# Performance work log

Measured on AMD Instinct MI355X. Metric: run time of the kernel, lower is better.

The kernel has to match this reference:

```python
import jax, jax.numpy as jnp
import numpy as np

B, C, R = 8, 256, 14
H_HEADS = 4
KD = 16            # key_dim
D_V = 64           # attn_ratio * key_dim
KS = 5             # dw conv kernel
N = R * R * R      # tokens


def _bias_idx():
    # replicate original offset logic: only first two coords (|dx|,|dy|) used
    pts = np.array(np.meshgrid(np.arange(R), np.arange(R), np.arange(R), indexing='ij'))
    pts = pts.reshape(3, -1).T  # (N, 3) in itertools.product order
    dx = np.abs(pts[:, 0:1] - pts[None, :, 0])  # (N, N)
    dy = np.abs(pts[:, 1:2] - pts[None, :, 1])
    return (dx * R + dy).astype(np.int32)  # (N, N), values in [0, R*R)


def setup_inputs() -> dict:
    key = jax.random.key(0)
    ks = jax.random.split(key, 12)
    cph = C // H_HEADS
    qkv_out = 2 * KD + D_V
    inp = {
        'x': jax.random.normal(ks[0], (B, C, R, R, R), jnp.float32),
        'Wqkv': jax.random.normal(ks[1], (H_HEADS, qkv_out, cph), jnp.float32) * 0.05,
        'qkv_scale': 1.0 + 0.05 * jax.random.normal(ks[2], (H_HEADS, qkv_out), jnp.float32),
        'qkv_bias': 0.05 * jax.random.normal(ks[3], (H_HEADS, qkv_out), jnp.float32),
        'Wdw': jax.random.normal(ks[4], (H_HEADS, KD, 1, KS, KS, KS), jnp.float32) * 0.05,
        'dw_scale': 1.0 + 0.05 * jax.random.normal(ks[5], (H_HEADS, KD), jnp.float32),
        'dw_bias': 0.05 * jax.random.normal(ks[6], (H_HEADS, KD), jnp.float32),
        'Wproj': jax.random.normal(ks[7], (C, D_V * H_HEADS), jnp.float32) * 0.02,
        'proj_scale': 1.0 + 0.05 * jax.random.normal(ks[8], (C,), jnp.float32),
        'proj_bias': 0.05 * jax.random.normal(ks[9], (C,), jnp.float32),
        'attention_biases': 0.02 * jax.random.normal(ks[10], (H_HEADS, R * R), jnp.float32),
        'bias_idx': jnp.asarray(_bias_idx()),
    }
    return inp


def reference(x, Wqkv, qkv_scale, qkv_bias, Wdw, dw_scale, dw_bias,
              Wproj, proj_scale, proj_bias, attention_biases, bias_idx):
    scale = KD ** (-0.5)
    ab = attention_biases[:, bias_idx]  # (h, N, N) relative-position bias gather
    feats_in = jnp.split(x, H_HEADS, axis=1)  # h x (B, C/h, R, R, R)
    dn = ('NCDHW', 'OIDHW', 'NCDHW')
    feats_out = []
    feat = feats_in[0]
    for i in range(H_HEADS):
        if i > 0:
            feat = feat + feats_in[i]
        # 1x1x1 conv QKV + fused BN (inference-style scale/shift)
        y = jnp.einsum('oc,bcxyz->boxyz', Wqkv[i], feat)
        y = y * qkv_scale[i][:, None, None, None] + qkv_bias[i][:, None, None, None]
        q = y[:, :KD]
        k = y[:, KD:2 * KD]
        v = y[:, 2 * KD:]
        # depthwise conv on q + fused BN
        q = jax.lax.conv_general_dilated(q, Wdw[i], (1, 1, 1), 'SAME',
                                         feature_group_count=KD, dimension_numbers=dn)
        q = q * dw_scale[i][:, None, None, None] + dw_bias[i][:, None, None, None]
        qf = q.reshape(B, KD, N)
        kf = k.reshape(B, KD, N)
        vf = v.reshape(B, D_V, N)
        attn = jnp.einsum('bcn,bcm->bnm', qf, kf) * scale + ab[i]  # (B, N, N)
        attn = jax.nn.softmax(attn, axis=-1)
        feat = jnp.einsum('bcm,bnm->bcn', vf, attn).reshape(B, D_V, R, R, R)
        feats_out.append(feat)
    h = jax.nn.relu(jnp.concatenate(feats_out, axis=1))  # (B, d*h, R, R, R)
    out = jnp.einsum('oc,bcxyz->boxyz', Wproj, h)
    out = out * proj_scale[:, None, None, None] + proj_bias[:, None, None, None]
    return out
```

## Files before the change

### kernel.cpp

```cpp
#include <hip/hip_runtime.h>

#define B_    8
#define C_    256
#define R_    14
#define R2    196
#define N3    2744
#define NP    2752
#define NH    4
#define KD    16
#define DV    64
#define QKVO  96
#define MT    64
#define NTILE 43
#define SPLIT 4
#define TPC   11

#define SC2   0.36067376f
#define LOG2E 1.44269504f

typedef __attribute__((ext_vector_type(8))) short short8v;
typedef __attribute__((ext_vector_type(4))) short short4v;
typedef __attribute__((ext_vector_type(4))) float float4v;

__device__ __forceinline__ int iabs(int v){ return v < 0 ? -v : v; }

__device__ __forceinline__ short f2bf(float f){
    union { float f; unsigned int u; } c; c.f = f;
    return (short)((c.u + 0x7FFFu + ((c.u >> 16) & 1u)) >> 16);
}
__device__ __forceinline__ float bf2f(short s){
    union { unsigned int u; float f; } c; c.u = ((unsigned int)(unsigned short)s) << 16;
    return c.f;
}

__global__ __launch_bounds__(256)
void wprep_kernel(const float* __restrict__ Wp, short* __restrict__ whi,
                  short* __restrict__ wlo, const float* __restrict__ Wqkv,
                  const float* __restrict__ qsc, short* __restrict__ wqhi,
                  short* __restrict__ wqlo)
{
    int i = blockIdx.x * 256 + threadIdx.x;
    {
        float w = Wp[i];
        short hi = f2bf(w);
        short lo = f2bf(w - bf2f(hi));
        whi[i] = hi; wlo[i] = lo;
    }
    if (i < NH * QKVO * 64) {
        int o_all = i >> 6;
        float w = Wqkv[i] * qsc[o_all];
        short hi = f2bf(w);
        short lo = f2bf(w - bf2f(hi));
        wqhi[i] = hi; wqlo[i] = lo;
    }
}

__global__ __launch_bounds__(256, 2)
void qkv_mfma(const float* __restrict__ x, float* __restrict__ h,
              const float* __restrict__ pacc, const float* __restrict__ pl,
              const short* __restrict__ wqhi, const short* __restrict__ wqlo,
              const float* __restrict__ qbi,
              float* __restrict__ q0, short* __restrict__ kbf, short* __restrict__ vbf,
              int head)
{
    __shared__ short fhi[64][72];
    __shared__ short flo[64][72];
    __shared__ float bsh[96];
    __shared__ float linv_s[64];

    const int b = blockIdx.y;
    const int n0 = blockIdx.x * 64;
    const int t = threadIdx.x;
    const int w = t >> 6, l = t & 63, g = l >> 4, ln = l & 15;

    if (t < 96) bsh[t] = qbi[head * QKVO + t];

    if (head > 0) {
        if (t < 64) {
            int n = n0 + t;
            float lt = pl[(size_t)(b * SPLIT + 0) * NP + n]
                     + pl[(size_t)(b * SPLIT + 1) * NP + n]
                     + pl[(size_t)(b * SPLIT + 2) * NP + n]
                     + pl[(size_t)(b * SPLIT + 3) * NP + n];
            linv_s[t] = 1.f / lt;
        }
        __syncthreads();
    }

    {
        const int sc_ = t & 63;
        const int sng = (t >> 6) * 16;
        const int nb = n0 + sng;
        const float* xs = x + ((size_t)b * C_ + head * DV + sc_) * N3 + nb;
        float fv[16];
        const bool fullblk = (nb + 15 < N3);
        if (fullblk) {
#pragma unroll
            for (int e4 = 0; e4 < 4; e4++) {
                float4 xv = ((const float4*)xs)[e4];
                fv[4*e4+0] = xv.x; fv[4*e4+1] = xv.y; fv[4*e4+2] = xv.z; fv[4*e4+3] = xv.w;
            }
        } else {
#pragma unroll
            for (int e = 0; e < 16; e++) fv[e] = (nb + e < N3) ? xs[e] : 0.f;
        }
        if (head > 0) {
            const float* pb = pacc + (size_t)b * SPLIT * DV * NP + (size_t)sc_ * NP + nb;
            float* hw = h + ((size_t)b * C_ + (head - 1) * DV + sc_) * N3 + nb;
            const size_t zs = (size_t)DV * NP;
            if (fullblk) {
#pragma unroll
                for (int e4 = 0; e4 < 4; e4++) {
                    float4 a0 = ((const float4*)(pb         ))[e4];
                    float4 a1 = ((const float4*)(pb +     zs))[e4];
                    float4 a2 = ((const float4*)(pb + 2 * zs))[e4];
                    float4 a3 = ((const float4*)(pb + 3 * zs))[e4];
                    float hc[4];
                    hc[0] = (a0.x + a1.x + a2.x + a3.x) * linv_s[sng + 4*e4 + 0];
                    hc[1] = (a0.y + a1.y + a2.y + a3.y) * linv_s[sng + 4*e4 + 1];
                    hc[2] = (a0.z + a1.z + a2.z + a3.z) * linv_s[sng + 4*e4 + 2];
                    hc[3] = (a0.w + a1.w + a2.w + a3.w) * linv_s[sng + 4*e4 + 3];
                    *(float4*)&hw[4*e4] = make_float4(hc[0], hc[1], hc[2], hc[3]);
                    fv[4*e4+0] += hc[0]; fv[4*e4+1] += hc[1];
                    fv[4*e4+2] += hc[2]; fv[4*e4+3] += hc[3];
                }
            } else {
#pragma unroll
                for (int e = 0; e < 16; e++) {
                    if (nb + e < N3) {
                        float a = pb[e] + pb[e + zs] + pb[e + 2*zs] + pb[e + 3*zs];
                        float hc = a * linv_s[sng + e];
                        hw[e] = hc;
                        fv[e] += hc;
                    }
                }
            }
        }
#pragma unroll
        for (int e = 0; e < 16; e++) {
            short hi = f2bf(fv[e]);
            short lo = f2bf(fv[e] - bf2f(hi));
            fhi[sng + e][sc_] = hi;
            flo[sng + e][sc_] = lo;
        }
    }
    __syncthreads();

    float4v acc[6];
#pragma unroll
    for (int os = 0; os < 6; os++) acc[os] = (float4v){0.f, 0.f, 0.f, 0.f};

    const short* wqh = wqhi + head * QKVO * 64;
    const short* wql = wqlo + head * QKVO * 64;
#pragma unroll
    for (int ck = 0; ck < 2; ck++) {
        short8v bh = *(const short8v*)&fhi[w * 16 + ln][ck * 32 + g * 8];
        short8v bl = *(const short8v*)&flo[w * 16 + ln][ck * 32 + g * 8];
#pragma unroll
        for (int os = 0; os < 6; os++) {
            size_t off = (size_t)(os * 16 + ln) * 64 + ck * 32 + g * 8;
            short8v wh = *(const short8v*)(wqh + off);
            short8v wl = *(const short8v*)(wql + off);
            acc[os] = __builtin_amdgcn_mfma_f32_16x16x32_bf16(wh, bh, acc[os], 0, 0, 0);
            acc[os] = __builtin_amdgcn_mfma_f32_16x16x32_bf16(wh, bl, acc[os], 0, 0, 0);
            acc[os] = __builtin_amdgcn_mfma_f32_16x16x32_bf16(wl, bh, acc[os], 0, 0, 0);
        }
    }

    const int n_ = n0 + w * 16 + ln;
    const bool ok = n_ < N3;
    float* qo = q0 + (size_t)b * KD * NP;
    short* ko = kbf + (size_t)b * NP * 16 + (size_t)n_ * 16;
    short* vo = vbf + (size_t)b * DV * NP;
#pragma unroll
    for (int os = 0; os < 6; os++) {
#pragma unroll
        for (int r = 0; r < 4; r++) {
            int o = os * 16 + g * 4 + r;
            float y = ok ? acc[os][r] + bsh[o] : 0.f;
            if (o < KD)            qo[(size_t)o * NP + n_] = y;
            else if (o < 2 * KD)   ko[o - KD] = f2bf(y);
            else                   vo[(size_t)(o - 2 * KD) * NP + n_] = f2bf(y);
        }
    }
}

__global__ __launch_bounds__(256)
void dwconv_kernel(float* __restrict__ q0, const float* __restrict__ Wdw,
                   const float* __restrict__ dsc, const float* __restrict__ dbi,
                   int head)
{
    __shared__ float pv[18 * 18 * 18];
    int b = blockIdx.y, c = blockIdx.x;
    int t = threadIdx.x;
    float* qc = q0 + ((size_t)b * KD + c) * NP;

    for (int i = t; i < 5832; i += 256) pv[i] = 0.f;
    __syncthreads();
    for (int i = t; i < N3; i += 256) {
        int xx = i / R2; int rem = i - xx * R2; int yy = rem / R_; int zz = rem - yy * R_;
        pv[(xx + 2) * 324 + (yy + 2) * 18 + (zz + 2)] = qc[i];
    }
    __syncthreads();

    const float* w = Wdw + (head * KD + c) * 125;
    float scl = dsc[head * KD + c], bia = dbi[head * KD + c];

    if (t < R2) {
        int x = t / R_, y = t - (t / R_) * R_;
        float acc[14];
#pragma unroll
        for (int z = 0; z < 14; z++) acc[z] = 0.f;
#pragma unroll
        for (int a = 0; a < 5; a++) {
#pragma unroll
            for (int bb = 0; bb < 5; bb++) {
                const float* base = &pv[(x + a) * 324 + (y + bb) * 18];
                float col[18];
#pragma unroll
                for (int j = 0; j < 18; j++) col[j] = base[j];
#pragma unroll
                for (int cc = 0; cc < 5; cc++) {
                    float wv = w[a * 25 + bb * 5 + cc];
#pragma unroll
                    for (int z = 0; z < 14; z++) acc[z] += wv * col[z + cc];
                }
            }
        }
        float* qo = qc + x * R2 + y * R_;
#pragma unroll
        for (int z = 0; z < 14; z++) qo[z] = acc[z] * scl + bia;
    }
}

__global__ __launch_bounds__(256, 6)
void attn_partial(const float* __restrict__ q0, const short* __restrict__ kbf,
                  const short* __restrict__ vbf, float* __restrict__ pacc,
                  float* __restrict__ pl, const float* __restrict__ abias, int head)
{
    __shared__ short ktT[64][40];
    __shared__ short vtT[64][72];
    __shared__ short plds[4][16][72];
    __shared__ int   mja[64];
    __shared__ float patch[6][8];

    const int b = blockIdx.y, z = blockIdx.z;
    const int qbase = blockIdx.x * 64;
    const int t = threadIdx.x;
    const int w = t >> 6;
    const int l = t & 63;
    const int g = l >> 4;
    const int ln = l & 15;

    const float* abh = abias + head * R2;
    const float* qq  = q0  + (size_t)b * KD * NP;
    const short* kbs = kbf + (size_t)b * NP * 16;
    const short* vbs = vbf + (size_t)b * DV * NP;

    {
        int mm = t & 63, dg = t >> 6;
        short4v zz = {0, 0, 0, 0};
        *(short4v*)&ktT[mm][16 + dg * 4] = zz;
    }

    const int n_my = qbase + w * 16 + ln;
    short8v qf;
#pragma unroll
    for (int j = 0; j < 8; j++) {
        int d = g * 8 + j;
        qf[j] = (d < KD) ? f2bf(qq[(size_t)d * NP + n_my]) : (short)0;
    }
    const int nxy0 = qbase / 14;
    const int njbase = (n_my / 14 - nxy0) * 8;

    float4v acc[4];
#pragma unroll
    for (int cs = 0; cs < 4; cs++) acc[cs] = (float4v){0.f, 0.f, 0.f, 0.f};
    float lsum = 0.f;

    const int smm = t >> 2, sq = t & 3;
    short4v kpre;
    short8v vpre0, vpre1;
    {
        const int m0 = (z * TPC) * MT;
        kpre = *(const short4v*)(kbs + (size_t)(m0 + smm) * 16 + sq * 4);
        const short* vs = vbs + (size_t)smm * NP + m0 + sq * 16;
        vpre0 = ((const short8v*)vs)[0];
        vpre1 = ((const short8v*)vs)[1];
    }

    const int tEnd = min(z * TPC + TPC, NTILE);
    for (int t0 = z * TPC; t0 < tEnd; t0++) {
        const int m0 = t0 * MT;
        __syncthreads();
        *(short4v*)&ktT[smm][sq * 4]      = kpre;
        *(short8v*)&vtT[smm][sq * 16]     = vpre0;
        *(short8v*)&vtT[smm][sq * 16 + 8] = vpre1;
        if (t < 64) {
            int m = m0 + t;
            mja[t] = (m < N3) ? (m / 14 - m0 / 14) : 6;
        } else if (t < 112) {
            int i = t - 64;
            int nj = i >> 3, mj = i & 7;
            float v = -20000.0f;
            if (mj < 6) {
                int nxy = nxy0 + nj;
                int mxy = m0 / 14 + mj;
                if (nxy < 196 && mxy < 196) {
                    int nx = nxy / 14, ny2 = nxy - nx * 14;
                    int mx = mxy / 14, my2 = mxy - mx * 14;
                    int idx = iabs(nx - mx) * 14 + iabs(ny2 - my2);
                    v = abh[idx] * LOG2E;
                }
            }
            patch[nj][mj] = v;
        }
        if (t0 + 1 < tEnd) {
            const int m1 = (t0 + 1) * MT;
            kpre = *(const short4v*)(kbs + (size_t)(m1 + smm) * 16 + sq * 4);
            const short* vs = vbs + (size_t)smm * NP + m1 + sq * 16;
            vpre0 = ((const short8v*)vs)[0];
            vpre1 = ((const short8v*)vs)[1];
        }
        __syncthreads();

        const float* pf = &patch[0][0];

#pragma unroll
        for (int ms = 0; ms < 4; ms++) {
            short8v af = *(const short8v*)&ktT[ms * 16 + ln][g * 8];
            float4v zf = {0.f, 0.f, 0.f, 0.f};
            float4v s = __builtin_amdgcn_mfma_f32_16x16x32_bf16(af, qf, zf, 0, 0, 0);
            int4 pk4 = *(const int4*)&mja[ms * 16 + g * 4];
            int pka[4] = {pk4.x, pk4.y, pk4.z, pk4.w};
            float p[4];
#pragma unroll
            for (int r = 0; r < 4; r++) {
                float bias = pf[njbase + pka[r]];
                float lg2 = fmaf(s[r], SC2, bias);
                p[r] = exp2f(lg2);
                lsum += p[r];
            }
            unsigned pk01, pk23;
            asm("v_cvt_pk_bf16_f32 %0, %1, %2" : "=v"(pk01) : "v"(p[0]), "v"(p[1]));
            asm("v_cvt_pk_bf16_f32 %0, %1, %2" : "=v"(pk23) : "v"(p[2]), "v"(p[3]));
            uint2 pw = make_uint2(pk01, pk23);
            *(uint2*)&plds[w][ln][ms * 16 + g * 4] = pw;
        }

#pragma unroll
        for (int ck = 0; ck < 2; ck++) {
            short8v pa = *(const short8v*)&plds[w][ln][ck * 32 + g * 8];
#pragma unroll
            for (int cs = 0; cs < 4; cs++) {
                short8v vf = *(const short8v*)&vtT[cs * 16 + ln][ck * 32 + g * 8];
                acc[cs] = __builtin_amdgcn_mfma_f32_16x16x32_bf16(pa, vf, acc[cs], 0, 0, 0);
            }
        }
    }

    lsum += __shfl_xor(lsum, 16);
    lsum += __shfl_xor(lsum, 32);

    float* pbase = pacc + (size_t)(b * SPLIT + z) * DV * NP;
    if (l < 16) {
        int n_l = qbase + w * 16 + l;
        if (n_l < N3) pl[(size_t)(b * SPLIT + z) * NP + n_l] = lsum;
    }
    const int n0w = qbase + w * 16 + g * 4;
    if (n0w < N3) {
#pragma unroll
        for (int cs = 0; cs < 4; cs++) {
            int c = cs * 16 + ln;
            *(float4v*)&pbase[(size_t)c * NP + n0w] = acc[cs];
        }
    }
}

__global__ __launch_bounds__(256, 2)
void proj_kernel(const float* __restrict__ h, const float* __restrict__ pacc,
                 const float* __restrict__ pl, const short* __restrict__ whi,
                 const short* __restrict__ wlo, const float* __restrict__ psc,
                 const float* __restrict__ pbi, float* __restrict__ out)
{
    __shared__ short hhi[64][40];
    __shared__ short hlo[64][40];
    __shared__ float linv_s[64];

    const int b = blockIdx.y;
    const int n0 = blockIdx.x * 64;
    const int t = threadIdx.x;
    const int w = t >> 6, l = t & 63, g = l >> 4, ln = l & 15;

    if (t < 64) {
        int n = n0 + t;
        float lt = pl[(size_t)(b * SPLIT + 0) * NP + n]
                 + pl[(size_t)(b * SPLIT + 1) * NP + n]
                 + pl[(size_t)(b * SPLIT + 2) * NP + n]
                 + pl[(size_t)(b * SPLIT + 3) * NP + n];
        linv_s[t] = 1.f / lt;
    }

    float4v acc[4][4];
#pragma unroll
    for (int os = 0; os < 4; os++)
#pragma unroll
        for (int ns = 0; ns < 4; ns++) acc[os][ns] = (float4v){0.f, 0.f, 0.f, 0.f};

    const float* hb = h + (size_t)b * C_ * N3;
    const int sc = t >> 3;
    const int sn = (t & 7) * 8;

    for (int c0 = 0; c0 < 256; c0 += 32) {
        __syncthreads();
        if (c0 < 192) {
            const float* hsrc = hb + (size_t)(c0 + sc) * N3 + n0 + sn;
            float4 f0 = ((const float4*)hsrc)[0];
            float4 f1 = ((const float4*)hsrc)[1];
            float va[8] = { f0.x, f0.y, f0.z, f0.w, f1.x, f1.y, f1.z, f1.w };
#pragma unroll
            for (int u = 0; u < 8; u++) {
                float v = va[u] > 0.f ? va[u] : 0.f;
                short hi = f2bf(v);
                short lo = f2bf(v - bf2f(hi));
                hhi[sn + u][sc] = hi;
                hlo[sn + u][sc] = lo;
            }
        } else {
            const int cl = c0 + sc - 192;
            const int nb = n0 + sn;
            const bool in = nb < N3;
            float va[8] = {0,0,0,0,0,0,0,0};
            if (in) {
                const float* pb = pacc + (size_t)b * SPLIT * DV * NP + (size_t)cl * NP + nb;
                const size_t zs = (size_t)DV * NP;
#pragma unroll
                for (int e4 = 0; e4 < 2; e4++) {
                    float4 a0 = ((const float4*)(pb         ))[e4];
                    float4 a1 = ((const float4*)(pb +     zs))[e4];
                    float4 a2 = ((const float4*)(pb + 2 * zs))[e4];
                    float4 a3 = ((const float4*)(pb + 3 * zs))[e4];
                    va[4*e4+0] = (a0.x + a1.x + a2.x + a3.x) * linv_s[sn + 4*e4 + 0];
                    va[4*e4+1] = (a0.y + a1.y + a2.y + a3.y) * linv_s[sn + 4*e4 + 1];
                    va[4*e4+2] = (a0.z + a1.z + a2.z + a3.z) * linv_s[sn + 4*e4 + 2];
                    va[4*e4+3] = (a0.w + a1.w + a2.w + a3.w) * linv_s[sn + 4*e4 + 3];
                }
            }
#pragma unroll
            for (int u = 0; u < 8; u++) {
                float v = va[u] > 0.f ? va[u] : 0.f;
                short hi = f2bf(v);
                short lo = f2bf(v - bf2f(hi));
                hhi[sn + u][sc] = hi;
                hlo[sn + u][sc] = lo;
            }
        }
        __syncthreads();

        short8v wh[4], wl[4];
#pragma unroll
        for (int os = 0; os < 4; os++) {
            size_t off = (size_t)(64 * w + os * 16 + ln) * 256 + c0 + g * 8;
            wh[os] = *(const short8v*)(whi + off);
            wl[os] = *(const short8v*)(wlo + off);
        }
#pragma unroll
        for (int ns = 0; ns < 4; ns++) {
            short8v bh = *(const short8v*)&hhi[ns * 16 + ln][g * 8];
            short8v bl = *(const short8v*)&hlo[ns * 16 + ln][g * 8];
#pragma unroll
            for (int os = 0; os < 4; os++) {
                acc[os][ns] = __builtin_amdgcn_mfma_f32_16x16x32_bf16(wh[os], bh, acc[os][ns], 0, 0, 0);
                acc[os][ns] = __builtin_amdgcn_mfma_f32_16x16x32_bf16(wh[os], bl, acc[os][ns], 0, 0, 0);
                acc[os][ns] = __builtin_amdgcn_mfma_f32_16x16x32_bf16(wl[os], bh, acc[os][ns], 0, 0, 0);
            }
        }
    }

    float* ob = out + (size_t)b * C_ * N3;
#pragma unroll
    for (int os = 0; os < 4; os++) {
#pragma unroll
        for (int r = 0; r < 4; r++) {
            int o = 64 * w + os * 16 + g * 4 + r;
            float s0 = psc[o], b0 = pbi[o];
#pragma unroll
            for (int ns = 0; ns < 4; ns++) {
                int n = n0 + ns * 16 + ln;
                if (n < N3) ob[(size_t)o * N3 + n] = acc[os][ns][r] * s0 + b0;
            }
        }
    }
}

extern "C" void kernel_launch(void* const* d_in, const int* in_sizes, int n_in,
                              void* d_out, int out_size, void* d_ws, size_t ws_size,
                              hipStream_t stream)
{
    const float* x    = (const float*)d_in[0];
    const float* Wqkv = (const float*)d_in[1];
    const float* qsc  = (const float*)d_in[2];
    const float* qbi  = (const float*)d_in[3];
    const float* Wdw  = (const float*)d_in[4];
    const float* dsc  = (const float*)d_in[5];
    const float* dbi  = (const float*)d_in[6];
    const float* Wp   = (const float*)d_in[7];
    const float* psc  = (const float*)d_in[8];
    const float* pbi  = (const float*)d_in[9];
    const float* ab   = (const float*)d_in[10];

    float* out = (float*)d_out;
    char*  wsb = (char*)d_ws;
    float* q0   = (float*)wsb;
    short* kbf  = (short*)(q0 + (size_t)B_ * KD * NP);
    short* vbf  = kbf + (size_t)B_ * NP * 16;
    float* h    = (float*)(vbf + (size_t)B_ * DV * NP);
    float* pacc = h + (size_t)B_ * C_ * N3;
    float* pl   = pacc + (size_t)B_ * SPLIT * DV * NP;
    short* whi  = (short*)(pl + (size_t)B_ * SPLIT * NP);
    short* wlo  = whi + 256 * 256;
    short* wqhi = wlo + 256 * 256;
    short* wqlo = wqhi + NH * QKVO * 64;

    wprep_kernel<<<256, 256, 0, stream>>>(Wp, whi, wlo, Wqkv, qsc, wqhi, wqlo);

    for (int head = 0; head < NH; head++) {
        qkv_mfma<<<dim3(43, B_), 256, 0, stream>>>(x, h, pacc, pl, wqhi, wqlo, qbi,
                                                   q0, kbf, vbf, head);
        dwconv_kernel<<<dim3(KD, B_), 256, 0, stream>>>(q0, Wdw, dsc, dbi, head);
        attn_partial<<<dim3(43, B_, SPLIT), 256, 0, stream>>>(q0, kbf, vbf, pacc, pl, ab, head);
    }
    proj_kernel<<<dim3(43, B_), 256, 0, stream>>>(h, pacc, pl, whi, wlo, psc, pbi, out);
}
```

Measured before the change: 315.2 us.

## Process two 64-query sub-tiles per attention block to reuse K/V tiles

Each attn_partial block now handles 128 queries (two 64-query sub-tiles per wave group) instead of 64, so every K/V tile staged in LDS feeds twice as many MFMAs. NP is padded to 2816 and NTILE to 44 so the larger tiles stay in bounds, the bias patch grows to 11 rows, and qkv_mfma gets 44 blocks. The aim is to halve global K/V loads and the per-tile sync and staging overhead. In exchange, register pressure rises (launch bounds drop to 4 waves per SIMD) and the attention grid shrinks to 22x8x4 blocks.

```diff
diff --git a/kernel.cpp b/kernel.cpp
--- a/kernel.cpp
+++ b/kernel.cpp
@@ -5,13 +5,13 @@
 #define R_    14
 #define R2    196
 #define N3    2744
-#define NP    2752
+#define NP    2816
 #define NH    4
 #define KD    16
 #define DV    64
 #define QKVO  96
 #define MT    64
-#define NTILE 43
+#define NTILE 44
 #define SPLIT 4
 #define TPC   11
 
@@ -233,19 +233,19 @@
     }
 }
 
-__global__ __launch_bounds__(256, 6)
+__global__ __launch_bounds__(256, 4)
 void attn_partial(const float* __restrict__ q0, const short* __restrict__ kbf,
                   const short* __restrict__ vbf, float* __restrict__ pacc,
                   float* __restrict__ pl, const float* __restrict__ abias, int head)
 {
     __shared__ short ktT[64][40];
     __shared__ short vtT[64][72];
-    __shared__ short plds[4][16][72];
+    __shared__ short plds[4][2][16][72];
     __shared__ int   mja[64];
-    __shared__ float patch[6][8];
+    __shared__ float patch[11][8];
 
     const int b = blockIdx.y, z = blockIdx.z;
-    const int qbase = blockIdx.x * 64;
+    const int qbase = blockIdx.x * 128;
     const int t = threadIdx.x;
     const int w = t >> 6;
     const int l = t & 63;
@@ -263,20 +263,26 @@
         *(short4v*)&ktT[mm][16 + dg * 4] = zz;
     }
 
-    const int n_my = qbase + w * 16 + ln;
-    short8v qf;
-#pragma unroll
-    for (int j = 0; j < 8; j++) {
-        int d = g * 8 + j;
-        qf[j] = (d < KD) ? f2bf(qq[(size_t)d * NP + n_my]) : (short)0;
-    }
     const int nxy0 = qbase / 14;
-    const int njbase = (n_my / 14 - nxy0) * 8;
-
-    float4v acc[4];
-#pragma unroll
-    for (int cs = 0; cs < 4; cs++) acc[cs] = (float4v){0.f, 0.f, 0.f, 0.f};
-    float lsum = 0.f;
+    int n_my[2], njb[2];
+    short8v qf[2];
+#pragma unroll
+    for (int sub = 0; sub < 2; sub++) {
+        n_my[sub] = qbase + sub * 64 + w * 16 + ln;
+#pragma unroll
+        for (int j = 0; j < 8; j++) {
+            int d = g * 8 + j;
+            qf[sub][j] = (d < KD) ? f2bf(qq[(size_t)d * NP + n_my[sub]]) : (short)0;
+        }
+        njb[sub] = (n_my[sub] / 14 - nxy0) * 8;
+    }
+
+    float4v acc[2][4];
+#pragma unroll
+    for (int sub = 0; sub < 2; sub++)
+#pragma unroll
+        for (int cs = 0; cs < 4; cs++) acc[sub][cs] = (float4v){0.f, 0.f, 0.f, 0.f};
+    float lsum[2] = {0.f, 0.f};
 
     const int smm = t >> 2, sq = t & 3;
     short4v kpre;
@@ -299,7 +305,7 @@
         if (t < 64) {
             int m = m0 + t;
             mja[t] = (m < N3) ? (m / 14 - m0 / 14) : 6;
-        } else if (t < 112) {
+        } else if (t < 152) {
             int i = t - 64;
             int nj = i >> 3, mj = i & 7;
             float v = -20000.0f;
@@ -329,50 +335,64 @@
 #pragma unroll
         for (int ms = 0; ms < 4; ms++) {
             short8v af = *(const short8v*)&ktT[ms * 16 + ln][g * 8];
-            float4v zf = {0.f, 0.f, 0.f, 0.f};
-            float4v s = __builtin_amdgcn_mfma_f32_16x16x32_bf16(af, qf, zf, 0, 0, 0);
             int4 pk4 = *(const int4*)&mja[ms * 16 + g * 4];
             int pka[4] = {pk4.x, pk4.y, pk4.z, pk4.w};
-            float p[4];
-#pragma unroll
-            for (int r = 0; r < 4; r++) {
-                float bias = pf[njbase + pka[r]];
-                float lg2 = fmaf(s[r], SC2, bias);
-                p[r] = exp2f(lg2);
-                lsum += p[r];
-            }
-            unsigned pk01, pk23;
-            asm("v_cvt_pk_bf16_f32 %0, %1, %2" : "=v"(pk01) : "v"(p[0]), "v"(p[1]));
-            asm("v_cvt_pk_bf16_f32 %0, %1, %2" : "=v"(pk23) : "v"(p[2]), "v"(p[3]));
-            uint2 pw = make_uint2(pk01, pk23);
-            *(uint2*)&plds[w][ln][ms * 16 + g * 4] = pw;
+#pragma unroll
+            for (int sub = 0; sub < 2; sub++) {
+                float4v zf = {0.f, 0.f, 0.f, 0.f};
+                float4v s = __builtin_amdgcn_mfma_f32_16x16x32_bf16(af, qf[sub], zf, 0, 0, 0);
+                float p[4];
+#pragma unroll
+                for (int r = 0; r < 4; r++) {
+                    float bias = pf[njb[sub] + pka[r]];
+                    float lg2 = fmaf(s[r], SC2, bias);
+                    p[r] = exp2f(lg2);
+                    lsum[sub] += p[r];
+                }
+                unsigned pk01, pk23;
+                asm("v_cvt_pk_bf16_f32 %0, %1, %2" : "=v"(pk01) : "v"(p[0]), "v"(p[1]));
+                asm("v_cvt_pk_bf16_f32 %0, %1, %2" : "=v"(pk23) : "v"(p[2]), "v"(p[3]));
+                uint2 pw = make_uint2(pk01, pk23);
+                *(uint2*)&plds[w][sub][ln][ms * 16 + g * 4] = pw;
+            }
         }
 
 #pragma unroll
         for (int ck = 0; ck < 2; ck++) {
-            short8v pa = *(const short8v*)&plds[w][ln][ck * 32 + g * 8];
+            short8v pa0 = *(const short8v*)&plds[w][0][ln][ck * 32 + g * 8];
+            short8v pa1 = *(const short8v*)&plds[w][1][ln][ck * 32 + g * 8];
 #pragma unroll
             for (int cs = 0; cs < 4; cs++) {
                 short8v vf = *(const short8v*)&vtT[cs * 16 + ln][ck * 32 + g * 8];
-                acc[cs] = __builtin_amdgcn_mfma_f32_16x16x32_bf16(pa, vf, acc[cs], 0, 0, 0);
-            }
-        }
-    }
-
-    lsum += __shfl_xor(lsum, 16);
-    lsum += __shfl_xor(lsum, 32);
+                acc[0][cs] = __builtin_amdgcn_mfma_f32_16x16x32_bf16(pa0, vf, acc[0][cs], 0, 0, 0);
+                acc[1][cs] = __builtin_amdgcn_mfma_f32_16x16x32_bf16(pa1, vf, acc[1][cs], 0, 0, 0);
+            }
+        }
+    }
+
+#pragma unroll
+    for (int sub = 0; sub < 2; sub++) {
+        lsum[sub] += __shfl_xor(lsum[sub], 16);
+        lsum[sub] += __shfl_xor(lsum[sub], 32);
+    }
 
     float* pbase = pacc + (size_t)(b * SPLIT + z) * DV * NP;
     if (l < 16) {
-        int n_l = qbase + w * 16 + l;
-        if (n_l < N3) pl[(size_t)(b * SPLIT + z) * NP + n_l] = lsum;
-    }
-    const int n0w = qbase + w * 16 + g * 4;
-    if (n0w < N3) {
-#pragma unroll
-        for (int cs = 0; cs < 4; cs++) {
-            int c = cs * 16 + ln;
-            *(float4v*)&pbase[(size_t)c * NP + n0w] = acc[cs];
+#pragma unroll
+        for (int sub = 0; sub < 2; sub++) {
+            int n_l = qbase + sub * 64 + w * 16 + l;
+            if (n_l < N3) pl[(size_t)(b * SPLIT + z) * NP + n_l] = lsum[sub];
+        }
+    }
+#pragma unroll
+    for (int sub = 0; sub < 2; sub++) {
+        const int n0w = qbase + sub * 64 + w * 16 + g * 4;
+        if (n0w < N3) {
+#pragma unroll
+            for (int cs = 0; cs < 4; cs++) {
+                int c = cs * 16 + ln;
+                *(float4v*)&pbase[(size_t)c * NP + n0w] = acc[sub][cs];
+            }
         }
     }
 }
@@ -525,10 +545,10 @@
     wprep_kernel<<<256, 256, 0, stream>>>(Wp, whi, wlo, Wqkv, qsc, wqhi, wqlo);
 
     for (int head = 0; head < NH; head++) {
-        qkv_mfma<<<dim3(43, B_), 256, 0, stream>>>(x, h, pacc, pl, wqhi, wqlo, qbi,
+        qkv_mfma<<<dim3(44, B_), 256, 0, stream>>>(x, h, pacc, pl, wqhi, wqlo, qbi,
                                                    q0, kbf, vbf, head);
         dwconv_kernel<<<dim3(KD, B_), 256, 0, stream>>>(q0, Wdw, dsc, dbi, head);
-        attn_partial<<<dim3(43, B_, SPLIT), 256, 0, stream>>>(q0, kbf, vbf, pacc, pl, ab, head);
+        attn_partial<<<dim3(22, B_, SPLIT), 256, 0, stream>>>(q0, kbf, vbf, pacc, pl, ab, head);
     }
     proj_kernel<<<dim3(43, B_), 256, 0, stream>>>(h, pacc, pl, whi, wlo, psc, pbi, out);
 }
```

New measurement: 339.6 us. 1.08x slower.
